# Performance work log

Hardware: AMD Instinct MI355X
Metric: run time of the kernel (lower is better)

## Reference

```python
import math
import jax, jax.numpy as jnp
import numpy as np

B, S, D, H = 2, 2048, 768, 12
DK = D // H

def setup_inputs() -> dict:
    key = jax.random.key(0)
    ks = jax.random.split(key, 8)
    scale = 1.0 / math.sqrt(D)
    return {
        "Q": jax.random.normal(ks[0], (B, S, D), dtype=jnp.float32),
        "K": jax.random.normal(ks[1], (B, S, D), dtype=jnp.float32),
        "V": jax.random.normal(ks[2], (B, S, D), dtype=jnp.float32),
        "mask": jax.random.randint(ks[3], (B, 1, S, S), 0, 2, dtype=jnp.int32),
        "W_Q": jax.random.normal(ks[4], (D, D), dtype=jnp.float32) * scale,
        "W_K": jax.random.normal(ks[5], (D, D), dtype=jnp.float32) * scale,
        "W_V": jax.random.normal(ks[6], (D, D), dtype=jnp.float32) * scale,
        "W_O": jax.random.normal(ks[7], (D, D), dtype=jnp.float32) * scale,
    }

def reference(Q, K, V, mask, W_Q, W_K, W_V, W_O):
    # torch Linear: y = x @ W.T (weight shape [out, in], no bias)
    q = (Q @ W_Q.T).reshape(B, S, H, DK).transpose(0, 2, 1, 3)  # [B,H,S,dk]
    k = (K @ W_K.T).reshape(B, S, H, DK).transpose(0, 2, 1, 3)
    v = (V @ W_V.T).reshape(B, S, H, DK).transpose(0, 2, 1, 3)
    scores = jnp.einsum('bhqd,bhkd->bhqk', q, k) / math.sqrt(DK)
    scores = jnp.where(mask == 0, -jnp.inf, scores)
    weights = jax.nn.softmax(scores, axis=-1)
    weights = jnp.nan_to_num(weights, nan=0.0)
    out = jnp.einsum('bhqk,bhkd->bhqd', weights, v)  # [B,H,S,dk]
    out = out.transpose(0, 2, 1, 3).reshape(B, S, D)
    return out @ W_O.T
```

## Files before the change

### kernel.cpp

```cpp
#include <hip/hip_runtime.h>
#include <hip/hip_bf16.h>
#include <stdint.h>

typedef __attribute__((ext_vector_type(8))) short bf16x8;
typedef __attribute__((ext_vector_type(4))) short bf16x4;
typedef __attribute__((ext_vector_type(4))) float f32x4;
typedef __attribute__((ext_vector_type(16))) float f32x16;
typedef __attribute__((ext_vector_type(4))) unsigned short u16x4;

__device__ __forceinline__ unsigned short f2bf(float x) {
  union { __hip_bfloat16 h; unsigned short s; } u;
  u.h = __float2bfloat16(x);
  return u.s;
}
__device__ __forceinline__ unsigned int cvtpk(float lo, float hi) {
  unsigned int r;
  asm("v_cvt_pk_bf16_f32 %0, %1, %2" : "=v"(r) : "v"(lo), "v"(hi));
  return r;
}
__device__ __forceinline__ void gll16(const unsigned short* g, unsigned short* l) {
  __builtin_amdgcn_global_load_lds(
      (const __attribute__((address_space(1))) unsigned int*)g,
      (__attribute__((address_space(3))) unsigned int*)l, 16, 0, 0);
}

__global__ __launch_bounds__(256) void prep_kernel(
    const int* __restrict__ mask, unsigned int* __restrict__ mp,
    const float* __restrict__ q, const float* __restrict__ k, const float* __restrict__ v,
    const float* __restrict__ wq, const float* __restrict__ wk, const float* __restrict__ wv,
    const float* __restrict__ wo,
    unsigned short* __restrict__ qb, unsigned short* __restrict__ kb, unsigned short* __restrict__ vb,
    unsigned short* __restrict__ wqb, unsigned short* __restrict__ wkb,
    unsigned short* __restrict__ wvb, unsigned short* __restrict__ wob) {
  if (blockIdx.x < 1024) {
    const int widx = blockIdx.x * 256 + threadIdx.x;
    const int* src = mask + (size_t)widx * 32;
    unsigned int wbits = 0;
#pragma unroll
    for (int j = 0; j < 8; ++j) {
      int4 vv = *(const int4*)(src + j * 4);
      wbits |= (vv.x != 0 ? 1u : 0u) << (j * 4 + 0);
      wbits |= (vv.y != 0 ? 1u : 0u) << (j * 4 + 1);
      wbits |= (vv.z != 0 ? 1u : 0u) << (j * 4 + 2);
      wbits |= (vv.w != 0 ? 1u : 0u) << (j * 4 + 3);
    }
    mp[widx] = wbits;
  } else {
    const int U = 1474560;
    const int stride = 2880 * 256;
    for (int u = (blockIdx.x - 1024) * 256 + threadIdx.x; u < U; u += stride) {
      const float* s; unsigned short* d; int r; float scale = 1.0f;
      if (u < 1179648) {
        int which = u / 393216; r = u - which * 393216;
        s = (which == 0) ? q : (which == 1) ? k : v;
        d = (which == 0) ? qb : (which == 1) ? kb : vb;
      } else {
        int u2 = u - 1179648; int which = u2 / 73728; r = u2 - which * 73728;
        s = (which == 0) ? wq : (which == 1) ? wk : (which == 2) ? wv : wo;
        d = (which == 0) ? wqb : (which == 1) ? wkb : (which == 2) ? wvb : wob;
        if (which == 0) scale = 0.18033688f;
      }
      float4 a = *(const float4*)&s[(size_t)r * 8];
      float4 b2 = *(const float4*)&s[(size_t)r * 8 + 4];
      uint4 o;
      o.x = cvtpk(a.x * scale, a.y * scale);
      o.y = cvtpk(a.z * scale, a.w * scale);
      o.z = cvtpk(b2.x * scale, b2.y * scale);
      o.w = cvtpk(b2.z * scale, b2.w * scale);
      *(uint4*)&d[(size_t)r * 8] = o;
    }
  }
}

__global__ __launch_bounds__(256) void maskpack_kernel(const int* __restrict__ mask,
                                                       unsigned int* __restrict__ mp,
                                                       int total) {
  int i = blockIdx.x * blockDim.x + threadIdx.x;
  const int lane = threadIdx.x & 63;
  const int stride = gridDim.x * blockDim.x;
  for (; i < total; i += stride) {
    unsigned long long b = __ballot(mask[i] != 0);
    if (lane == 0)       mp[i >> 5] = (unsigned int)b;
    else if (lane == 32) mp[i >> 5] = (unsigned int)(b >> 32);
  }
}

#define GEMM_BODY(AEXPR, BEXPR)                                                   \
  __shared__ unsigned short As[3][128][32];                                       \
  __shared__ unsigned short Bs[3][128][32];                                       \
  const int m0 = blockIdx.y * 128, n0 = blockIdx.x * 128;                         \
  const int t = threadIdx.x, lane = t & 63, w = t >> 6;                           \
  const int wr = w >> 1, wc = w & 1, fr = lane & 15, cl = lane >> 4;              \
  const int srl = lane >> 2, sph = lane & 3;                                      \
  f32x4 acc[4][4] = {};                                                           \
  auto ISSUE = [&](int kk, int buf) {                                             \
    _Pragma("unroll")                                                             \
    for (int i = 0; i < 2; ++i) {                                                 \
      const int row = i * 64 + w * 16 + srl;                                      \
      const int c = sph ^ ((row >> 1) & 3);                                       \
      gll16(AEXPR, &As[buf][i * 64 + w * 16][0]);                                 \
      gll16(BEXPR, &Bs[buf][i * 64 + w * 16][0]);                                 \
    }                                                                             \
  };                                                                              \
  ISSUE(0, 0);                                                                    \
  ISSUE(32, 1);                                                                   \
  asm volatile("s_waitcnt vmcnt(4)" ::: "memory");                                \
  __syncthreads();                                                                \
  for (int it = 0; it < 24; ++it) {                                               \
    const int buf = it - (it / 3) * 3;                                            \
    if (it < 22) {                                                                \
      const int nb = (it + 2) - ((it + 2) / 3) * 3;                               \
      ISSUE((it + 2) * 32, nb);                                                   \
    }                                                                             \
    bf16x8 af[4], bfr[4];                                                         \
    _Pragma("unroll")                                                             \
    for (int i = 0; i < 4; ++i) {                                                 \
      const int R = wr * 64 + i * 16 + fr;                                        \
      af[i] = *(const bf16x8*)&As[buf][R][(cl ^ ((R >> 1) & 3)) * 8];             \
    }                                                                             \
    _Pragma("unroll")                                                             \
    for (int j = 0; j < 4; ++j) {                                                 \
      const int R = wc * 64 + j * 16 + fr;                                        \
      bfr[j] = *(const bf16x8*)&Bs[buf][R][(cl ^ ((R >> 1) & 3)) * 8];            \
    }                                                                             \
    __builtin_amdgcn_s_setprio(1);                                                \
    _Pragma("unroll")                                                             \
    for (int i = 0; i < 4; ++i)                                                   \
      _Pragma("unroll")                                                           \
      for (int j = 0; j < 4; ++j)                                                 \
        acc[i][j] = __builtin_amdgcn_mfma_f32_16x16x32_bf16(af[i], bfr[j],        \
                                                            acc[i][j], 0, 0, 0); \
    __builtin_amdgcn_s_setprio(0);                                                \
    if (it < 22) asm volatile("s_waitcnt vmcnt(4)" ::: "memory");                 \
    else         asm volatile("s_waitcnt vmcnt(0)" ::: "memory");                 \
    __syncthreads();                                                              \
  }

__global__ __launch_bounds__(256) void proj_b16(
    const unsigned short* __restrict__ Qb, const unsigned short* __restrict__ Kb,
    const unsigned short* __restrict__ Vb,
    const unsigned short* __restrict__ Wqb, const unsigned short* __restrict__ Wkb,
    const unsigned short* __restrict__ Wvb,
    unsigned short* __restrict__ qo, unsigned short* __restrict__ ko,
    unsigned short* __restrict__ vo) {
  const int z = blockIdx.z;
  const unsigned short* A = (z == 0) ? Qb : (z == 1) ? Kb : Vb;
  const unsigned short* W = (z == 0) ? Wqb : (z == 1) ? Wkb : Wvb;
  GEMM_BODY(A + (size_t)(m0 + row) * 768 + kk + c * 8,
            W + (size_t)(n0 + row) * 768 + kk + c * 8)
  if (z == 2) {
    for (int i = 0; i < 4; ++i)
      for (int j = 0; j < 4; ++j) {
        int m = m0 + wr * 64 + i * 16 + (lane >> 4) * 4;
        int n = n0 + wc * 64 + j * 16 + fr;
        int b = m >> 11, s = m & 2047, hd = n >> 6, dk = n & 63;
        u16x4 pk;
        for (int r = 0; r < 4; ++r) pk[r] = f2bf(acc[i][j][r]);
        *(u16x4*)&vo[((size_t)(b * 12 + hd) * 64 + dk) * 2048 + s] = pk;
      }
  } else {
    unsigned short* O = (z == 0) ? qo : ko;
    for (int i = 0; i < 4; ++i)
      for (int j = 0; j < 4; ++j)
        for (int r = 0; r < 4; ++r) {
          int m = m0 + wr * 64 + i * 16 + (lane >> 4) * 4 + r;
          int n = n0 + wc * 64 + j * 16 + fr;
          int b = m >> 11, s = m & 2047, hd = n >> 6, dk = n & 63;
          O[((size_t)(b * 12 + hd) * 2048 + s) * 64 + dk] = f2bf(acc[i][j][r]);
        }
  }
}

__global__ __launch_bounds__(256) void out_b16(
    const unsigned short* __restrict__ Ain, const unsigned short* __restrict__ Wob,
    float* __restrict__ Out) {
  GEMM_BODY(Ain + (size_t)(m0 + row) * 768 + kk + c * 8,
            Wob + (size_t)(n0 + row) * 768 + kk + c * 8)
  for (int i = 0; i < 4; ++i)
    for (int j = 0; j < 4; ++j)
      for (int r = 0; r < 4; ++r) {
        int m = m0 + wr * 64 + i * 16 + (lane >> 4) * 4 + r;
        int n = n0 + wc * 64 + j * 16 + fr;
        Out[(size_t)m * 768 + n] = acc[i][j][r];
      }
}

__global__ __launch_bounds__(256) void proj_gemm(
    const float* __restrict__ Qi, const float* __restrict__ Ki, const float* __restrict__ Vi,
    const float* __restrict__ Wq, const float* __restrict__ Wk, const float* __restrict__ Wv,
    unsigned short* __restrict__ qo, unsigned short* __restrict__ ko, unsigned short* __restrict__ vo) {
  constexpr int LDT = 56;
  __shared__ unsigned short As[128][LDT];
  __shared__ unsigned short Bs[128][LDT];
  const int z = blockIdx.z;
  const float* A = (z == 0) ? Qi : (z == 1) ? Ki : Vi;
  const float* W = (z == 0) ? Wq : (z == 1) ? Wk : Wv;
  const int m0 = blockIdx.y * 128, n0 = blockIdx.x * 128;
  const int t = threadIdx.x, lane = t & 63, w = t >> 6;
  const int wr = w >> 1, wc = w & 1;
  const int fr = lane & 15, fg = (lane >> 4) * 8;
  const int srow = t >> 3, sseg = t & 7;
  f32x4 acc[4][4] = {};
  for (int kk = 0; kk < 768; kk += 32) {
    for (int pp = 0; pp < 4; ++pp) {
      int row = srow + pp * 32;
      float4 fa = *(const float4*)&A[(size_t)(m0 + row) * 768 + kk + sseg * 4];
      float4 fb = *(const float4*)&W[(size_t)(n0 + row) * 768 + kk + sseg * 4];
      bf16x4 pa = {(short)f2bf(fa.x), (short)f2bf(fa.y), (short)f2bf(fa.z), (short)f2bf(fa.w)};
      bf16x4 pb = {(short)f2bf(fb.x), (short)f2bf(fb.y), (short)f2bf(fb.z), (short)f2bf(fb.w)};
      *(bf16x4*)&As[row][sseg * 4] = pa;
      *(bf16x4*)&Bs[row][sseg * 4] = pb;
    }
    __syncthreads();
    bf16x8 af[4], bfr[4];
    for (int i = 0; i < 4; ++i) af[i]  = *(const bf16x8*)&As[wr * 64 + i * 16 + fr][fg];
    for (int i = 0; i < 4; ++i) bfr[i] = *(const bf16x8*)&Bs[wc * 64 + i * 16 + fr][fg];
    for (int i = 0; i < 4; ++i)
      for (int j = 0; j < 4; ++j)
        acc[i][j] = __builtin_amdgcn_mfma_f32_16x16x32_bf16(af[i], bfr[j], acc[i][j], 0, 0, 0);
    __syncthreads();
  }
  if (z == 2) {
    for (int i = 0; i < 4; ++i)
      for (int j = 0; j < 4; ++j) {
        int m = m0 + wr * 64 + i * 16 + (lane >> 4) * 4;
        int n = n0 + wc * 64 + j * 16 + fr;
        int b = m >> 11, s = m & 2047, hd = n >> 6, dk = n & 63;
        u16x4 pk;
        for (int r = 0; r < 4; ++r) pk[r] = f2bf(acc[i][j][r]);
        *(u16x4*)&vo[((size_t)(b * 12 + hd) * 64 + dk) * 2048 + s] = pk;
      }
  } else {
    unsigned short* O = (z == 0) ? qo : ko;
    const float scale = (z == 0) ? 0.18033688f : 1.0f;
    for (int i = 0; i < 4; ++i)
      for (int j = 0; j < 4; ++j)
        for (int r = 0; r < 4; ++r) {
          int m = m0 + wr * 64 + i * 16 + (lane >> 4) * 4 + r;
          int n = n0 + wc * 64 + j * 16 + fr;
          int b = m >> 11, s = m & 2047, hd = n >> 6, dk = n & 63;
          O[((size_t)(b * 12 + hd) * 2048 + s) * 64 + dk] = f2bf(acc[i][j][r] * scale);
        }
  }
}

__global__ __launch_bounds__(256) void out_gemm(
    const unsigned short* __restrict__ Ain, const float* __restrict__ W,
    float* __restrict__ Out) {
  constexpr int LDT = 56;
  __shared__ unsigned short As[128][LDT];
  __shared__ unsigned short Bs[128][LDT];
  const int m0 = blockIdx.y * 128, n0 = blockIdx.x * 128;
  const int t = threadIdx.x, lane = t & 63, w = t >> 6;
  const int wr = w >> 1, wc = w & 1;
  const int fr = lane & 15, fg = (lane >> 4) * 8;
  f32x4 acc[4][4] = {};
  for (int kk = 0; kk < 768; kk += 32) {
    {
      int row = t >> 2, seg = t & 3;
      for (int pp = 0; pp < 2; ++pp) {
        bf16x8 va = *(const bf16x8*)&Ain[(size_t)(m0 + row + pp * 64) * 768 + kk + seg * 8];
        *(bf16x8*)&As[row + pp * 64][seg * 8] = va;
      }
      int row2 = t >> 3, seg2 = t & 7;
      for (int pp = 0; pp < 4; ++pp) {
        float4 fb = *(const float4*)&W[(size_t)(n0 + row2 + pp * 32) * 768 + kk + seg2 * 4];
        bf16x4 pb = {(short)f2bf(fb.x), (short)f2bf(fb.y), (short)f2bf(fb.z), (short)f2bf(fb.w)};
        *(bf16x4*)&Bs[row2 + pp * 32][seg2 * 4] = pb;
      }
    }
    __syncthreads();
    bf16x8 af[4], bfr[4];
    for (int i = 0; i < 4; ++i) af[i]  = *(const bf16x8*)&As[wr * 64 + i * 16 + fr][fg];
    for (int i = 0; i < 4; ++i) bfr[i] = *(const bf16x8*)&Bs[wc * 64 + i * 16 + fr][fg];
    for (int i = 0; i < 4; ++i)
      for (int j = 0; j < 4; ++j)
        acc[i][j] = __builtin_amdgcn_mfma_f32_16x16x32_bf16(af[i], bfr[j], acc[i][j], 0, 0, 0);
    __syncthreads();
  }
  for (int i = 0; i < 4; ++i)
    for (int j = 0; j < 4; ++j)
      for (int r = 0; r < 4; ++r) {
        int m = m0 + wr * 64 + i * 16 + (lane >> 4) * 4 + r;
        int n = n0 + wc * 64 + j * 16 + fr;
        Out[(size_t)m * 768 + n] = acc[i][j][r];
      }
}

__global__ __launch_bounds__(512) void attn_kernel(
    const unsigned short* __restrict__ qh, const unsigned short* __restrict__ kh,
    const unsigned short* __restrict__ vh, const unsigned int* __restrict__ mp,
    unsigned short* __restrict__ ao) {
  __shared__ union LdsU {
    struct {
      unsigned short K[2][4][32][64];
      unsigned short V[2][4][64][32];
    } st;
    float M[8][32][64];
  } lds;
  __shared__ float Sm[8][64];
  __shared__ float Sl[8][64];
  const int t = threadIdx.x, lane = t & 63, w = t >> 6;
  const int wq = w & 1, sp = w >> 1;
  const int bid = blockIdx.x;
  const int xcd = bid & 7, idx = bid >> 3;
  const int bh = xcd * 3 + (idx >> 5);
  const int qb = idx & 31;
  const int bb = bh / 12, hh = bh % 12;
  const int qc = lane & 31, h = lane >> 5;
  const int q = qb * 64 + wq * 32 + qc;
  const unsigned short* qrow = qh + ((size_t)bh * 2048 + q) * 64;
  bf16x8 bq[4];
#pragma unroll
  for (int kc = 0; kc < 4; ++kc) bq[kc] = *(const bf16x8*)(qrow + kc * 16 + h * 8);
  const unsigned int* mrow = mp + ((size_t)bb * 2048 + q) * 64 + sp * 16;
  const unsigned short* kgb = kh + (size_t)bh * 2048 * 64;
  const unsigned short* vgb = vh + (size_t)bh * 64 * 2048;
  f32x16 acc0 = {}, acc1 = {};
  float l_run = 0.f;
  float m_run = -1e30f;
  const int KT0 = sp * 512;
  const int krow = lane >> 3, ksch = (lane & 7) ^ (lane >> 3);
  const int vrow = lane >> 2, vsch = (lane & 3) ^ ((lane >> 3) & 3);
  auto ISSUE = [&](int it2, int b2) {
    const int KT = KT0 + it2 * 32;
    unsigned short* kd = &lds.st.K[b2][sp][0][0];
    unsigned short* vd = &lds.st.V[b2][sp][0][0];
#pragma unroll
    for (int c2 = 0; c2 < 2; ++c2) {
      const int c = 2 * wq + c2;
      gll16(kgb + (size_t)(KT + c * 8 + krow) * 64 + ksch * 8, kd + c * 512);
    }
#pragma unroll
    for (int c2 = 0; c2 < 2; ++c2) {
      const int c = 2 * wq + c2;
      gll16(vgb + (size_t)(c * 16 + vrow) * 2048 + KT + vsch * 8, vd + c * 512);
    }
  };
  ISSUE(0, 0);
#pragma unroll 2
  for (int it = 0; it < 16; ++it) {
    const int b = it & 1;
    asm volatile("s_waitcnt vmcnt(0)" ::: "memory");
    __syncthreads();
    if (it < 15) ISSUE(it + 1, b ^ 1);
    const unsigned int m32 = mrow[it];
    bf16x8 ka[4];
#pragma unroll
    for (int kc = 0; kc < 4; ++kc)
      ka[kc] = *(const bf16x8*)&lds.st.K[b][sp][qc][((kc * 2 + h) ^ (qc & 7)) * 8];
    f32x16 sc = {};
    __builtin_amdgcn_s_setprio(1);
#pragma unroll
    for (int kc = 0; kc < 4; ++kc)
      sc = __builtin_amdgcn_mfma_f32_32x32x16_bf16(ka[kc], bq[kc], sc, 0, 0, 0);
    __builtin_amdgcn_s_setprio(0);
    bf16x8 va0[2], va1[2];
#pragma unroll
    for (int ks = 0; ks < 2; ++ks) {
      const int cs = ((ks * 2 + h) ^ ((qc >> 1) & 3)) * 8;
      va0[ks] = *(const bf16x8*)&lds.st.V[b][sp][qc][cs];
      va1[ks] = *(const bf16x8*)&lds.st.V[b][sp][32 + qc][cs];
    }
    const unsigned int wsh = m32 >> (4 * h);
#pragma unroll
    for (int r = 0; r < 16; ++r) {
      const int sh = (r & 3) + 8 * (r >> 2);
      sc[r] = ((wsh >> sh) & 1u) ? sc[r] : -3.0e38f;
    }
    float mA0 = fmaxf(fmaxf(sc[0], sc[4]), fmaxf(sc[8], sc[12]));
    float mA1 = fmaxf(fmaxf(sc[1], sc[5]), fmaxf(sc[9], sc[13]));
    float mA2 = fmaxf(fmaxf(sc[2], sc[6]), fmaxf(sc[10], sc[14]));
    float mA3 = fmaxf(fmaxf(sc[3], sc[7]), fmaxf(sc[11], sc[15]));
    float m1 = fmaxf(fmaxf(mA0, mA1), fmaxf(mA2, mA3));
    float tmax = fmaxf(m1, __shfl_xor(m1, 32, 64));
    if (__any(tmax > m_run + 8.0f)) {
      float mnew = fmaxf(m_run, tmax);
      float scl = exp2f(m_run - mnew);
      m_run = mnew;
      l_run *= scl;
#pragma unroll
      for (int e = 0; e < 16; ++e) { acc0[e] *= scl; acc1[e] *= scl; }
    }
#pragma unroll
    for (int r = 0; r < 16; ++r) sc[r] = exp2f(sc[r] - m_run);
    float sA0 = (sc[0] + sc[4]) + (sc[8] + sc[12]);
    float sA1 = (sc[1] + sc[5]) + (sc[9] + sc[13]);
    float sA2 = (sc[2] + sc[6]) + (sc[10] + sc[14]);
    float sA3 = (sc[3] + sc[7]) + (sc[11] + sc[15]);
    float s1 = (sA0 + sA1) + (sA2 + sA3);
    l_run += s1 + __shfl_xor(s1, 32, 64);
    __builtin_amdgcn_s_setprio(1);
#define PVQ(P, OFF, A0, A1) { \
    unsigned int a0 = cvtpk(P[OFF + 0], P[OFF + 1]), a1 = cvtpk(P[OFF + 2], P[OFF + 3]); \
    unsigned int b0 = cvtpk(P[OFF + 4], P[OFF + 5]), b1 = cvtpk(P[OFF + 6], P[OFF + 7]); \
    asm("v_permlane32_swap_b32 %0, %1" : "+v"(a0), "+v"(b0)); \
    asm("v_permlane32_swap_b32 %0, %1" : "+v"(a1), "+v"(b1)); \
    union { unsigned int u[4]; bf16x8 v; } bfu; \
    bfu.u[0] = a0; bfu.u[1] = a1; bfu.u[2] = b0; bfu.u[3] = b1; \
    acc0 = __builtin_amdgcn_mfma_f32_32x32x16_bf16(A0, bfu.v, acc0, 0, 0, 0); \
    acc1 = __builtin_amdgcn_mfma_f32_32x32x16_bf16(A1, bfu.v, acc1, 0, 0, 0); }
    PVQ(sc, 0, va0[0], va1[0]);
    PVQ(sc, 8, va0[1], va1[1]);
#undef PVQ
    __builtin_amdgcn_s_setprio(0);
  }
  __syncthreads();
  Sm[w][lane] = m_run;
  Sl[w][lane] = l_run;
#pragma unroll
  for (int e = 0; e < 16; ++e) lds.M[w][e][lane] = acc0[e];
#pragma unroll
  for (int e = 0; e < 16; ++e) lds.M[w][16 + e][lane] = acc1[e];
  __syncthreads();
  float pm0 = Sm[wq][lane],     pm1 = Sm[2 + wq][lane];
  float pm2 = Sm[4 + wq][lane], pm3 = Sm[6 + wq][lane];
  float M = fmaxf(fmaxf(pm0, pm1), fmaxf(pm2, pm3));
  float w0 = exp2f(pm0 - M), w1 = exp2f(pm1 - M), w2 = exp2f(pm2 - M), w3 = exp2f(pm3 - M);
  float L = Sl[wq][lane] * w0 + Sl[2 + wq][lane] * w1 +
            Sl[4 + wq][lane] * w2 + Sl[6 + wq][lane] * w3;
  float inv = (L > 0.f) ? 1.0f / L : 0.f;
  unsigned short* orow = ao + ((size_t)bb * 2048 + q) * 768 + hh * 64;
#pragma unroll
  for (int g = 0; g < 2; ++g) {
    const int e0 = sp * 8 + g * 4;
    const int base = (e0 >= 16) ? 32 : 0;
    const int er0 = e0 & 15;
    const int d0 = base + 8 * (er0 >> 2) + 4 * h;
    u16x4 pk4;
#pragma unroll
    for (int j = 0; j < 4; ++j) {
      float v = (lds.M[wq][e0 + j][lane] * w0 + lds.M[2 + wq][e0 + j][lane] * w1 +
                 lds.M[4 + wq][e0 + j][lane] * w2 + lds.M[6 + wq][e0 + j][lane] * w3) * inv;
      pk4[j] = f2bf(v);
    }
    *(u16x4*)&orow[d0] = pk4;
  }
}

extern "C" void kernel_launch(void* const* d_in, const int* in_sizes, int n_in,
                              void* d_out, int out_size, void* d_ws, size_t ws_size,
                              hipStream_t stream) {
  const float* Q  = (const float*)d_in[0];
  const float* K  = (const float*)d_in[1];
  const float* V  = (const float*)d_in[2];
  const int*   mask = (const int*)d_in[3];
  const float* WQ = (const float*)d_in[4];
  const float* WK = (const float*)d_in[5];
  const float* WV = (const float*)d_in[6];
  const float* WO = (const float*)d_in[7];
  float* out = (float*)d_out;
  char* ws = (char*)d_ws;

  const size_t NEED = 43515904ull;
  if (ws_size >= NEED) {
    unsigned short* qh  = (unsigned short*)(ws + 0);
    unsigned short* kh  = (unsigned short*)(ws + 6291456);
    unsigned short* vh  = (unsigned short*)(ws + 12582912);
    unsigned int*   mp  = (unsigned int*)(ws + 18874368);
    unsigned short* Qb  = (unsigned short*)(ws + 19922944);
    unsigned short* ao  = Qb;
    unsigned short* Kb  = (unsigned short*)(ws + 26214400);
    unsigned short* Vb  = (unsigned short*)(ws + 32505856);
    unsigned short* Wqb = (unsigned short*)(ws + 38797312);
    unsigned short* Wkb = (unsigned short*)(ws + 39976960);
    unsigned short* Wvb = (unsigned short*)(ws + 41156608);
    unsigned short* Wob = (unsigned short*)(ws + 42336256);
    prep_kernel<<<dim3(3904), 256, 0, stream>>>(mask, mp, Q, K, V, WQ, WK, WV, WO,
                                                Qb, Kb, Vb, Wqb, Wkb, Wvb, Wob);
    proj_b16<<<dim3(6, 32, 3), 256, 0, stream>>>(Qb, Kb, Vb, Wqb, Wkb, Wvb, qh, kh, vh);
    attn_kernel<<<dim3(768), 512, 0, stream>>>(qh, kh, vh, mp, ao);
    out_b16<<<dim3(6, 32), 256, 0, stream>>>(ao, Wob, out);
  } else {
    unsigned short* qh = (unsigned short*)(ws + 0);
    unsigned short* kh = (unsigned short*)(ws + 6291456);
    unsigned short* vh = (unsigned short*)(ws + 12582912);
    unsigned short* ao = (unsigned short*)(ws + 18874368);
    unsigned int*   mp = (unsigned int*)(ws + 25165824);
    maskpack_kernel<<<dim3(2048), 256, 0, stream>>>(mask, mp, 2 * 2048 * 2048);
    proj_gemm<<<dim3(6, 32, 3), 256, 0, stream>>>(Q, K, V, WQ, WK, WV, qh, kh, vh);
    attn_kernel<<<dim3(768), 512, 0, stream>>>(qh, kh, vh, mp, ao);
    out_gemm<<<dim3(6, 32), 256, 0, stream>>>(ao, WO, out);
  }
}
```

Before: 144.9 us.

## Use 1024-thread attention blocks with 128 queries and four KV splits

Adds an attention kernel variant in which each 1024-thread block handles 128 query rows with four key-range splits (16 waves), replacing the 512-thread, 64-query-row version on the main path. K/V tiles loaded into LDS are shared by four query-row waves instead of two, which halves the number of blocks and the redundant K/V traffic. The cost is larger blocks with possibly lower occupancy and a heavier cross-wave merge of partial results through LDS at the end.

```diff
diff --git a/kernel.cpp b/kernel.cpp
--- a/kernel.cpp
+++ b/kernel.cpp
@@ -287,6 +287,169 @@
       }
 }
 
+__global__ __launch_bounds__(1024) void attn16_kernel(
+    const unsigned short* __restrict__ qh, const unsigned short* __restrict__ kh,
+    const unsigned short* __restrict__ vh, const unsigned int* __restrict__ mp,
+    unsigned short* __restrict__ ao) {
+  __shared__ union LdsU {
+    struct {
+      unsigned short K[2][4][32][64];
+      unsigned short V[2][4][64][32];
+    } st;
+    float M16[16][16][64];
+  } lds;
+  __shared__ float Sm[16][64];
+  __shared__ float Sl[16][64];
+  const int t = threadIdx.x, lane = t & 63, w = t >> 6;
+  const int wq = w & 3, sp = w >> 2;
+  const int bid = blockIdx.x;
+  const int xcd = bid & 7, idx = bid >> 3;
+  const int bh = xcd * 3 + (idx >> 4);
+  const int qb = idx & 15;
+  const int bb = bh / 12, hh = bh % 12;
+  const int qc = lane & 31, h = lane >> 5;
+  const int q = qb * 128 + wq * 32 + qc;
+  const unsigned short* qrow = qh + ((size_t)bh * 2048 + q) * 64;
+  bf16x8 bq[4];
+#pragma unroll
+  for (int kc = 0; kc < 4; ++kc) bq[kc] = *(const bf16x8*)(qrow + kc * 16 + h * 8);
+  const unsigned int* mrow = mp + ((size_t)bb * 2048 + q) * 64 + sp * 16;
+  const unsigned short* kgb = kh + (size_t)bh * 2048 * 64;
+  const unsigned short* vgb = vh + (size_t)bh * 64 * 2048;
+  f32x16 acc0 = {}, acc1 = {};
+  float l_run = 0.f;
+  float m_run = -1e30f;
+  const int KT0 = sp * 512;
+  const int krow = lane >> 3, ksch = (lane & 7) ^ (lane >> 3);
+  const int vrow = lane >> 2, vsch = (lane & 3) ^ ((lane >> 3) & 3);
+  auto ISSUE = [&](int it2, int b2) {
+    const int KT = KT0 + it2 * 32;
+    unsigned short* kd = &lds.st.K[b2][sp][0][0];
+    unsigned short* vd = &lds.st.V[b2][sp][0][0];
+    const int c = wq;
+    gll16(kgb + (size_t)(KT + c * 8 + krow) * 64 + ksch * 8, kd + c * 512);
+    gll16(vgb + (size_t)(c * 16 + vrow) * 2048 + KT + vsch * 8, vd + c * 512);
+  };
+  ISSUE(0, 0);
+#pragma unroll 2
+  for (int it = 0; it < 16; ++it) {
+    const int b = it & 1;
+    asm volatile("s_waitcnt vmcnt(0)" ::: "memory");
+    __syncthreads();
+    if (it < 15) ISSUE(it + 1, b ^ 1);
+    const unsigned int m32 = mrow[it];
+    bf16x8 ka[4];
+#pragma unroll
+    for (int kc = 0; kc < 4; ++kc)
+      ka[kc] = *(const bf16x8*)&lds.st.K[b][sp][qc][((kc * 2 + h) ^ (qc & 7)) * 8];
+    f32x16 sc = {};
+    __builtin_amdgcn_s_setprio(1);
+#pragma unroll
+    for (int kc = 0; kc < 4; ++kc)
+      sc = __builtin_amdgcn_mfma_f32_32x32x16_bf16(ka[kc], bq[kc], sc, 0, 0, 0);
+    __builtin_amdgcn_s_setprio(0);
+    bf16x8 va0[2], va1[2];
+#pragma unroll
+    for (int ks = 0; ks < 2; ++ks) {
+      const int cs = ((ks * 2 + h) ^ ((qc >> 1) & 3)) * 8;
+      va0[ks] = *(const bf16x8*)&lds.st.V[b][sp][qc][cs];
+      va1[ks] = *(const bf16x8*)&lds.st.V[b][sp][32 + qc][cs];
+    }
+    const unsigned int wsh = m32 >> (4 * h);
+#pragma unroll
+    for (int r = 0; r < 16; ++r) {
+      const int sh = (r & 3) + 8 * (r >> 2);
+      sc[r] = ((wsh >> sh) & 1u) ? sc[r] : -3.0e38f;
+    }
+    float mA0 = fmaxf(fmaxf(sc[0], sc[4]), fmaxf(sc[8], sc[12]));
+    float mA1 = fmaxf(fmaxf(sc[1], sc[5]), fmaxf(sc[9], sc[13]));
+    float mA2 = fmaxf(fmaxf(sc[2], sc[6]), fmaxf(sc[10], sc[14]));
+    float mA3 = fmaxf(fmaxf(sc[3], sc[7]), fmaxf(sc[11], sc[15]));
+    float m1 = fmaxf(fmaxf(mA0, mA1), fmaxf(mA2, mA3));
+    float tmax = fmaxf(m1, __shfl_xor(m1, 32, 64));
+    if (__any(tmax > m_run + 8.0f)) {
+      float mnew = fmaxf(m_run, tmax);
+      float scl = exp2f(m_run - mnew);
+      m_run = mnew;
+      l_run *= scl;
+#pragma unroll
+      for (int e = 0; e < 16; ++e) { acc0[e] *= scl; acc1[e] *= scl; }
+    }
+#pragma unroll
+    for (int r = 0; r < 16; ++r) sc[r] = exp2f(sc[r] - m_run);
+    float sA0 = (sc[0] + sc[4]) + (sc[8] + sc[12]);
+    float sA1 = (sc[1] + sc[5]) + (sc[9] + sc[13]);
+    float sA2 = (sc[2] + sc[6]) + (sc[10] + sc[14]);
+    float sA3 = (sc[3] + sc[7]) + (sc[11] + sc[15]);
+    float s1 = (sA0 + sA1) + (sA2 + sA3);
+    l_run += s1 + __shfl_xor(s1, 32, 64);
+    __builtin_amdgcn_s_setprio(1);
+#define PVQ(P, OFF, A0, A1) { \
+    unsigned int a0 = cvtpk(P[OFF + 0], P[OFF + 1]), a1 = cvtpk(P[OFF + 2], P[OFF + 3]); \
+    unsigned int b0 = cvtpk(P[OFF + 4], P[OFF + 5]), b1 = cvtpk(P[OFF + 6], P[OFF + 7]); \
+    asm("v_permlane32_swap_b32 %0, %1" : "+v"(a0), "+v"(b0)); \
+    asm("v_permlane32_swap_b32 %0, %1" : "+v"(a1), "+v"(b1)); \
+    union { unsigned int u[4]; bf16x8 v; } bfu; \
+    bfu.u[0] = a0; bfu.u[1] = a1; bfu.u[2] = b0; bfu.u[3] = b1; \
+    acc0 = __builtin_amdgcn_mfma_f32_32x32x16_bf16(A0, bfu.v, acc0, 0, 0, 0); \
+    acc1 = __builtin_amdgcn_mfma_f32_32x32x16_bf16(A1, bfu.v, acc1, 0, 0, 0); }
+    PVQ(sc, 0, va0[0], va1[0]);
+    PVQ(sc, 8, va0[1], va1[1]);
+#undef PVQ
+    __builtin_amdgcn_s_setprio(0);
+  }
+  __syncthreads();
+  Sm[w][lane] = m_run;
+  Sl[w][lane] = l_run;
+#pragma unroll
+  for (int e = 0; e < 16; ++e) lds.M16[w][e][lane] = acc0[e];
+  __syncthreads();
+  float pm0 = Sm[wq][lane],     pm1 = Sm[4 + wq][lane];
+  float pm2 = Sm[8 + wq][lane], pm3 = Sm[12 + wq][lane];
+  float M = fmaxf(fmaxf(pm0, pm1), fmaxf(pm2, pm3));
+  float w0 = exp2f(pm0 - M), w1 = exp2f(pm1 - M), w2 = exp2f(pm2 - M), w3 = exp2f(pm3 - M);
+  float L = Sl[wq][lane] * w0 + Sl[4 + wq][lane] * w1 +
+            Sl[8 + wq][lane] * w2 + Sl[12 + wq][lane] * w3;
+  float inv = (L > 0.f) ? 1.0f / L : 0.f;
+  unsigned short* orow = ao + ((size_t)bb * 2048 + q) * 768 + hh * 64;
+  if (sp < 2) {
+    const int e0 = sp * 8;
+#pragma unroll
+    for (int g = 0; g < 2; ++g) {
+      u16x4 pk4;
+#pragma unroll
+      for (int j = 0; j < 4; ++j) {
+        const int e = e0 + g * 4 + j;
+        float v = (lds.M16[wq][e][lane] * w0 + lds.M16[4 + wq][e][lane] * w1 +
+                   lds.M16[8 + wq][e][lane] * w2 + lds.M16[12 + wq][e][lane] * w3) * inv;
+        pk4[j] = f2bf(v);
+      }
+      const int d0 = 8 * ((e0 + g * 4) >> 2) + 4 * h;
+      *(u16x4*)&orow[d0] = pk4;
+    }
+  }
+  __syncthreads();
+#pragma unroll
+  for (int e = 0; e < 16; ++e) lds.M16[w][e][lane] = acc1[e];
+  __syncthreads();
+  if (sp >= 2) {
+    const int e0 = (sp - 2) * 8;
+#pragma unroll
+    for (int g = 0; g < 2; ++g) {
+      u16x4 pk4;
+#pragma unroll
+      for (int j = 0; j < 4; ++j) {
+        const int e = e0 + g * 4 + j;
+        float v = (lds.M16[wq][e][lane] * w0 + lds.M16[4 + wq][e][lane] * w1 +
+                   lds.M16[8 + wq][e][lane] * w2 + lds.M16[12 + wq][e][lane] * w3) * inv;
+        pk4[j] = f2bf(v);
+      }
+      const int d0 = 32 + 8 * ((e0 + g * 4) >> 2) + 4 * h;
+      *(u16x4*)&orow[d0] = pk4;
+    }
+  }
+}
+
 __global__ __launch_bounds__(512) void attn_kernel(
     const unsigned short* __restrict__ qh, const unsigned short* __restrict__ kh,
     const unsigned short* __restrict__ vh, const unsigned int* __restrict__ mp,
@@ -469,7 +632,7 @@
     prep_kernel<<<dim3(3904), 256, 0, stream>>>(mask, mp, Q, K, V, WQ, WK, WV, WO,
                                                 Qb, Kb, Vb, Wqb, Wkb, Wvb, Wob);
     proj_b16<<<dim3(6, 32, 3), 256, 0, stream>>>(Qb, Kb, Vb, Wqb, Wkb, Wvb, qh, kh, vh);
-    attn_kernel<<<dim3(768), 512, 0, stream>>>(qh, kh, vh, mp, ao);
+    attn16_kernel<<<dim3(384), 1024, 0, stream>>>(qh, kh, vh, mp, ao);
     out_b16<<<dim3(6, 32), 256, 0, stream>>>(ao, Wob, out);
   } else {
     unsigned short* qh = (unsigned short*)(ws + 0);
```

Measured after the change: 169.3 us. 1.17x slower.
